# Performance work log

Hardware: AMD Instinct MI355X
Metric: run time of the kernel (lower is better)

The kernel has to match this reference:

```python
import jax, jax.numpy as jnp
import numpy as np

DIM = 1024
NUM_HEADS = 16
HEAD_DIM = DIM // NUM_HEADS
MAX_LEN = 2048
ROPE_BASE = 10000.0


def _rope_tables(n, d, base=ROPE_BASE):
    inv_freq = 1.0 / (base ** (np.arange(0, d, 2, dtype=np.float32) / d))  # [d/2]
    t = np.arange(n, dtype=np.float32)
    freqs = np.outer(t, inv_freq)  # [n, d/2]
    return jnp.asarray(np.cos(freqs)), jnp.asarray(np.sin(freqs))


def _apply_rotary(x, cos, sin):
    # x: [B, H, N, D]; pairs are consecutive elements (2i, 2i+1)
    xe = x[..., 0::2]
    xo = x[..., 1::2]
    # cos/sin: [N, D/2] -> broadcast over B, H
    oe = xe * cos - xo * sin
    oo = xe * sin + xo * cos
    return jnp.stack([oe, oo], axis=-1).reshape(x.shape)


def setup_inputs() -> dict:
    key = jax.random.key(0)
    ks = jax.random.split(key, 11)
    B, T, S = 4, 2048, 2048
    sc = 1.0 / np.sqrt(DIM)
    inp = {
        "query": jax.random.normal(ks[0], (B, T, DIM), jnp.float32),
        "key": jax.random.normal(ks[1], (B, S, DIM), jnp.float32),
        "value": jax.random.normal(ks[2], (B, S, DIM), jnp.float32),
        "Wq": jax.random.normal(ks[3], (DIM, DIM), jnp.float32) * sc,
        "bq": jnp.zeros((DIM,), jnp.float32),
        "Wk": jax.random.normal(ks[4], (DIM, DIM), jnp.float32) * sc,
        "bk": jnp.zeros((DIM,), jnp.float32),
        "Wv": jax.random.normal(ks[5], (DIM, DIM), jnp.float32) * sc,
        "bv": jnp.zeros((DIM,), jnp.float32),
        "Wo": jax.random.normal(ks[6], (DIM, DIM), jnp.float32) * sc,
        "bo": jnp.zeros((DIM,), jnp.float32),
    }
    return inp


def reference(query, key, value, Wq, bq, Wk, bk, Wv, bv, Wo, bo):
    B, T, C = query.shape
    S = key.shape[1]
    H, D = NUM_HEADS, HEAD_DIM
    scale = D ** -0.5

    q = (query @ Wq + bq).reshape(B, T, H, D).transpose(0, 2, 1, 3)  # [B,H,T,D]
    k = (key @ Wk + bk).reshape(B, S, H, D).transpose(0, 2, 1, 3)    # [B,H,S,D]
    v = (value @ Wv + bv).reshape(B, S, H, D).transpose(0, 2, 1, 3)  # [B,H,S,D]

    cos, sin = _rope_tables(max(T, S), D)
    q = _apply_rotary(q, cos[:T], sin[:T])
    k = _apply_rotary(k, cos[:S], sin[:S])

    scores = jnp.einsum("bhtd,bhsd->bhts", q, k) * scale  # [B,H,T,S]
    causal = jnp.tril(jnp.ones((T, S), bool))
    scores = jnp.where(causal[None, None], scores, -jnp.inf)
    att = jax.nn.softmax(scores, axis=-1)

    out = jnp.einsum("bhts,bhsd->bhtd", att, v)  # [B,H,T,D]
    out = out.transpose(0, 2, 1, 3).reshape(B, T, C)
    return out @ Wo + bo
```

## Files before the change

### kernel.cpp

```cpp
#include <hip/hip_runtime.h>
#include <cstdint>
#include <math.h>

typedef __bf16 bf16_t;
typedef __bf16 bf16x8 __attribute__((ext_vector_type(8)));
typedef __bf16 bf16x4 __attribute__((ext_vector_type(4)));
typedef float f32x4 __attribute__((ext_vector_type(4)));

#define MFMA16(a, b, c) __builtin_amdgcn_mfma_f32_16x16x32_bf16((a), (b), (c), 0, 0, 0)

static constexpr int BATCH = 4;
static constexpr int SEQ = 2048;
static constexpr int DIMC = 1024;
static constexpr int NH = 16;
static constexpr int HD = 64;

__device__ __forceinline__ void async_copy16(void* lds, const void* g) {
    __builtin_amdgcn_global_load_lds(
        (const __attribute__((address_space(1))) void*)g,
        (__attribute__((address_space(3))) void*)lds, 16, 0, 0);
}

__device__ __forceinline__ float fast_exp2(float x) {
#if __has_builtin(__builtin_amdgcn_exp2f)
    return __builtin_amdgcn_exp2f(x);
#else
    return __expf(x * 0.6931471805599453f);
#endif
}

__global__ __launch_bounds__(256) void cvt3(const float* __restrict__ q,
                                            const float* __restrict__ k,
                                            const float* __restrict__ v,
                                            bf16_t* __restrict__ out) {
    const float* in = (blockIdx.y == 0) ? q : ((blockIdx.y == 1) ? k : v);
    bf16_t* o = out + (size_t)blockIdx.y * BATCH * SEQ * DIMC;
    const int i = blockIdx.x * 256 + threadIdx.x;
    const float4 f0 = ((const float4*)in)[i * 2];
    const float4 f1 = ((const float4*)in)[i * 2 + 1];
    bf16x8 vv;
    vv[0] = (bf16_t)f0.x; vv[1] = (bf16_t)f0.y; vv[2] = (bf16_t)f0.z; vv[3] = (bf16_t)f0.w;
    vv[4] = (bf16_t)f1.x; vv[5] = (bf16_t)f1.y; vv[6] = (bf16_t)f1.z; vv[7] = (bf16_t)f1.w;
    ((bf16x8*)o)[i] = vv;
}

__global__ __launch_bounds__(256) void transpose_cvt(const float* __restrict__ W0,
                                                     const float* __restrict__ W1,
                                                     const float* __restrict__ W2,
                                                     const float* __restrict__ W3,
                                                     bf16_t* __restrict__ out) {
    const float* Ws[4] = {W0, W1, W2, W3};
    const float* W = Ws[blockIdx.z];
    bf16_t* Wt = out + (size_t)blockIdx.z * DIMC * DIMC;
    __shared__ float tile[32][33];
    const int tx = threadIdx.x & 31;
    const int ty = threadIdx.x >> 5;
    const int x0 = blockIdx.x * 32;
    const int y0 = blockIdx.y * 32;
    #pragma unroll
    for (int j = ty; j < 32; j += 8)
        tile[j][tx] = W[(size_t)(y0 + j) * DIMC + x0 + tx];
    __syncthreads();
    #pragma unroll
    for (int j = ty; j < 32; j += 8)
        Wt[(size_t)(x0 + j) * DIMC + y0 + tx] = (bf16_t)tile[tx][j];
}

__global__ __launch_bounds__(256) void rope_tab(float* __restrict__ cosT, float* __restrict__ sinT) {
    const int idx = blockIdx.x * 256 + threadIdx.x;
    const int t = idx >> 5;
    const int p = idx & 31;
    const float inv = exp2f(-0.41524101186092029f * (float)p);
    const float ang = (float)t * inv;
    float s, c;
    sincosf(ang, &s, &c);
    cosT[idx] = c;
    sinT[idx] = s;
}

template <int MI>
__device__ __forceinline__ void gemm_core(const bf16_t* __restrict__ A,
                                          const bf16_t* __restrict__ Bt,
                                          const int row0, const int col0,
                                          bf16_t* As, bf16_t* Bs, const int tid,
                                          f32x4 (&acc)[MI][4]) {
    constexpr int ABUF = MI * 32 * 32;
    constexpr int BBUF = 256 * 32;
    constexpr int NT = DIMC / 32;
    const int wid = tid >> 6;
    const int lane = tid & 63;
    const int l15 = lane & 15;
    const int quad = lane >> 4;
    const int wr = wid >> 2;
    const int wc = wid & 3;
    const int rIn = lane >> 2;
    const int gW = ((lane & 3) ^ ((rIn & 3) ^ ((rIn >> 2) & 3))) * 8;
    const int fR = (l15 & 3) ^ ((l15 >> 2) & 3);

#define STAGE_TILE(bi, kt)                                                              \
    {                                                                                   \
        const int k0_ = (kt)*32;                                                        \
        bf16_t* as_ = As + (bi)*ABUF;                                                   \
        bf16_t* bs_ = Bs + (bi)*BBUF;                                                   \
        if constexpr (MI == 8) {                                                        \
            _Pragma("unroll") for (int ci = 0; ci < 2; ++ci) {                          \
                const int c = 2 * wid + ci;                                             \
                async_copy16(&as_[c * 512],                                             \
                             A + (size_t)(row0 + c * 16 + rIn) * DIMC + k0_ + gW);      \
            }                                                                           \
        } else {                                                                        \
            async_copy16(&as_[wid * 512],                                               \
                         A + (size_t)(row0 + wid * 16 + rIn) * DIMC + k0_ + gW);        \
        }                                                                               \
        _Pragma("unroll") for (int ci = 0; ci < 2; ++ci) {                              \
            const int c = 2 * wid + ci;                                                 \
            async_copy16(&bs_[c * 512],                                                 \
                         Bt + (size_t)(col0 + c * 16 + rIn) * DIMC + k0_ + gW);         \
        }                                                                               \
    }

    STAGE_TILE(0, 0)
    STAGE_TILE(1, 1)
    int rb = 0;
    for (int t = 0; t < NT; ++t) {
        if (t == NT - 1) {
            asm volatile("s_waitcnt vmcnt(0)" ::: "memory");
        } else {
            if constexpr (MI == 8)
                asm volatile("s_waitcnt vmcnt(4)" ::: "memory");
            else
                asm volatile("s_waitcnt vmcnt(3)" ::: "memory");
        }
        asm volatile("s_barrier" ::: "memory");
        if (t + 2 < NT) {
            int sb = rb + 2;
            if (sb >= 3) sb -= 3;
            STAGE_TILE(sb, t + 2)
        }
        const bf16_t* as = As + rb * ABUF;
        const bf16_t* bs = Bs + rb * BBUF;
        bf16x8 bfrag[4];
        #pragma unroll
        for (int ni = 0; ni < 4; ++ni)
            bfrag[ni] = *(const bf16x8*)&bs[(wc * 64 + ni * 16 + l15) * 32 + ((quad ^ fR) << 3)];
        bf16x8 afrag[MI];
        #pragma unroll
        for (int mi = 0; mi < MI; ++mi)
            afrag[mi] =
                *(const bf16x8*)&as[(wr * (MI * 16) + mi * 16 + l15) * 32 + ((quad ^ fR) << 3)];
        __builtin_amdgcn_s_setprio(1);
        #pragma unroll
        for (int mi = 0; mi < MI; ++mi)
            #pragma unroll
            for (int ni = 0; ni < 4; ++ni)
                acc[mi][ni] = MFMA16(afrag[mi], bfrag[ni], acc[mi][ni]);
        __builtin_amdgcn_s_setprio(0);
        rb = rb + 1 == 3 ? 0 : rb + 1;
    }
#undef STAGE_TILE
}

__global__ __launch_bounds__(512, 2) void gemm_qkv(const bf16_t* __restrict__ Cb,
                                                   const bf16_t* __restrict__ Wt3,
                                                   const float* __restrict__ bq,
                                                   const float* __restrict__ bk,
                                                   const float* __restrict__ bv,
                                                   bf16_t* __restrict__ Qr,
                                                   bf16_t* __restrict__ Kr,
                                                   bf16_t* __restrict__ Vr,
                                                   const float* __restrict__ cosT,
                                                   const float* __restrict__ sinT) {
    __shared__ __align__(16) unsigned char smem[98304];
    bf16_t* As = (bf16_t*)smem;
    bf16_t* Bs = (bf16_t*)(smem + 49152);
    float* eps = (float*)smem;
    const int z = blockIdx.z;
    const bf16_t* A = Cb + (size_t)z * BATCH * SEQ * DIMC;
    const bf16_t* Bt = Wt3 + (size_t)z * DIMC * DIMC;
    const float* bias = (z == 0) ? bq : ((z == 1) ? bk : bv);
    bf16_t* outp = (z == 0) ? Qr : ((z == 1) ? Kr : Vr);
    const bool rope = (z < 2);
    const int tid = threadIdx.x;
    const int row0 = blockIdx.y * 256, col0 = blockIdx.x * 256;
    f32x4 acc[8][4] = {};
    gemm_core<8>(A, Bt, row0, col0, As, Bs, tid, acc);

    const int wid = tid >> 6;
    const int lane = tid & 63;
    const int l15 = lane & 15;
    const int quad = lane >> 4;
    const int wr = wid >> 2, wc = wid & 3;
    float bvl[4];
    #pragma unroll
    for (int ni = 0; ni < 4; ++ni) bvl[ni] = bias[col0 + wc * 64 + ni * 16 + l15];
    const int lr = tid >> 4;
    const int cg = tid & 15;
    const int c0 = cg * 16;
    const int h = (col0 + c0) >> 6;
    const int dbase = c0 & 63;
    const float osc = (z == 0) ? 0.18033688011112043f : 1.0f;
    #pragma unroll
    for (int p = 0; p < 8; ++p) {
        __syncthreads();
        #pragma unroll
        for (int ni = 0; ni < 4; ++ni)
            #pragma unroll
            for (int r = 0; r < 4; ++r)
                eps[(wr * 16 + quad * 4 + r) * 264 + wc * 64 + ni * 16 + l15] =
                    acc[p][ni][r] + bvl[ni];
        __syncthreads();
        const int grow = row0 + (lr >> 4) * 128 + p * 16 + (lr & 15);
        const int tq = grow & (SEQ - 1);
        const int bb = grow >> 11;
        float vals[16];
        #pragma unroll
        for (int q4 = 0; q4 < 4; ++q4) {
            f32x4 vv = *(const f32x4*)&eps[lr * 264 + c0 + q4 * 4];
            vals[q4 * 4 + 0] = vv[0]; vals[q4 * 4 + 1] = vv[1];
            vals[q4 * 4 + 2] = vv[2]; vals[q4 * 4 + 3] = vv[3];
        }
        bf16x8 o0, o1;
        if (rope) {
            const int pbase = tq * 32 + (dbase >> 1);
            const float4 cs0 = *(const float4*)&cosT[pbase];
            const float4 cs1 = *(const float4*)&cosT[pbase + 4];
            const float4 sn0 = *(const float4*)&sinT[pbase];
            const float4 sn1 = *(const float4*)&sinT[pbase + 4];
            const float cc[8] = {cs0.x, cs0.y, cs0.z, cs0.w, cs1.x, cs1.y, cs1.z, cs1.w};
            const float ss[8] = {sn0.x, sn0.y, sn0.z, sn0.w, sn1.x, sn1.y, sn1.z, sn1.w};
            #pragma unroll
            for (int i = 0; i < 8; ++i) {
                const float e = vals[2 * i], o = vals[2 * i + 1];
                const float oe = (e * cc[i] - o * ss[i]) * osc;
                const float oo = (e * ss[i] + o * cc[i]) * osc;
                if (i < 4) { o0[2 * i] = (bf16_t)oe; o0[2 * i + 1] = (bf16_t)oo; }
                else { o1[2 * (i - 4)] = (bf16_t)oe; o1[2 * (i - 4) + 1] = (bf16_t)oo; }
            }
        } else {
            #pragma unroll
            for (int i = 0; i < 8; ++i) o0[i] = (bf16_t)vals[i];
            #pragma unroll
            for (int i = 0; i < 8; ++i) o1[i] = (bf16_t)vals[8 + i];
        }
        bf16_t* dst = outp + (((size_t)bb * NH + h) * SEQ + tq) * HD + dbase;
        *(bf16x8*)dst = o0;
        *(bf16x8*)(dst + 8) = o1;
    }
}

__global__ __launch_bounds__(512, 2) void gemm_o(const bf16_t* __restrict__ A,
                                                 const bf16_t* __restrict__ Bt,
                                                 const float* __restrict__ bias,
                                                 float* __restrict__ out) {
    __shared__ __align__(16) unsigned char smem[73728];
    bf16_t* As = (bf16_t*)smem;
    bf16_t* Bs = (bf16_t*)(smem + 24576);
    const int tid = threadIdx.x;
    const int row0 = blockIdx.y * 128, col0 = blockIdx.x * 256;
    f32x4 acc[4][4] = {};
    gemm_core<4>(A, Bt, row0, col0, As, Bs, tid, acc);
    const int wid = tid >> 6;
    const int lane = tid & 63;
    const int l15 = lane & 15;
    const int quad = lane >> 4;
    const int wr = wid >> 2, wc = wid & 3;
    #pragma unroll
    for (int ni = 0; ni < 4; ++ni) {
        const int col = col0 + wc * 64 + ni * 16 + l15;
        const float bvl = bias[col];
        #pragma unroll
        for (int mi = 0; mi < 4; ++mi) {
            #pragma unroll
            for (int r = 0; r < 4; ++r) {
                const int row = row0 + wr * 64 + mi * 16 + quad * 4 + r;
                out[(size_t)row * DIMC + col] = acc[mi][ni][r] + bvl;
            }
        }
    }
}

__global__ __launch_bounds__(256) void attn_kernel(const bf16_t* __restrict__ Qr,
                                                   const bf16_t* __restrict__ Kr,
                                                   const bf16_t* __restrict__ Vr,
                                                   bf16_t* __restrict__ O) {
    __shared__ bf16_t Ks[2][64 * 64];
    __shared__ bf16_t Vt[2][64 * 72];
    __shared__ bf16_t Ps[4][32 * 72];
    const int tid = threadIdx.x;
    const int w = tid >> 6;
    const int lane = tid & 63;
    const int l15 = lane & 15;
    const int quad = lane >> 4;
    const int bh = blockIdx.x;
    const int b = bh >> 4, h = bh & 15;
    const bf16_t* Qb = Qr + (size_t)bh * SEQ * HD;
    const bf16_t* Kb = Kr + (size_t)bh * SEQ * HD;
    const bf16_t* Vb = Vr + (size_t)bh * SEQ * HD;

    bf16x8 ones;
    #pragma unroll
    for (int j8 = 0; j8 < 8; ++j8) ones[j8] = (bf16_t)1.0f;
    bf16x8 idB[2];
    #pragma unroll
    for (int ch = 0; ch < 2; ++ch)
        #pragma unroll
        for (int j8 = 0; j8 < 8; ++j8)
            idB[ch][j8] = (quad * 8 + j8 == ch * 16 + l15) ? (bf16_t)1.0f : (bf16_t)0.0f;

    const int sIn = lane >> 3;
    const int gK = ((lane & 7) ^ sIn) * 8;
    const int fK = (l15 & 7);

#define VTRANS(buf, a0, a1)                                                      \
    {                                                                            \
        _Pragma("unroll") for (int c = 0; c < 4; ++c) {                          \
            f32x4 zt = {};                                                       \
            f32x4 tv = MFMA16((c < 2) ? (a0) : (a1), idB[c & 1], zt);            \
            bf16x4 pkt;                                                          \
            _Pragma("unroll") for (int rr = 0; rr < 4; ++rr)                     \
                pkt[rr] = (bf16_t)tv[rr];                                        \
            *(bf16x4*)&Vt[buf][(c * 16 + l15) * 72 + w * 16 + quad * 4] = pkt;   \
        }                                                                        \
    }

    const int j = 15 - (int)blockIdx.y;
    const int q0 = j * 128;
    bf16x8 qa[2][2];
    #pragma unroll
    for (int mg = 0; mg < 2; ++mg)
        #pragma unroll
        for (int kc = 0; kc < 2; ++kc)
            qa[mg][kc] = *(const bf16x8*)(Qb + (size_t)(q0 + mg * 64 + w * 16 + l15) * HD +
                                          kc * 32 + quad * 8);
    f32x4 acco[2][4] = {};
    f32x4 accl[2] = {};
    const int nIter = 2 * j + 2;

    #pragma unroll
    for (int ci = 0; ci < 2; ++ci) {
        const int c = 2 * w + ci;
        async_copy16(&Ks[0][c * 512], Kb + (size_t)(c * 8 + sIn) * HD + gK);
    }
    {
        const bf16_t* vsrc = Vb + (size_t)(w * 16 + l15) * HD + quad * 8;
        bf16x8 pv0 = *(const bf16x8*)vsrc;
        bf16x8 pv1 = *(const bf16x8*)(vsrc + 32);
        VTRANS(0, pv0, pv1);
    }
    __syncthreads();

    int cur = 0;
    for (int it = 0; it < nIter; ++it) {
        const int nxt = cur ^ 1;
        const bool hn = (it + 1 < nIter);
        bf16x8 av0, av1;
        if (hn) {
            const int s1 = (it + 1) * 64;
            #pragma unroll
            for (int ci = 0; ci < 2; ++ci) {
                const int c = 2 * w + ci;
                async_copy16(&Ks[nxt][c * 512], Kb + (size_t)(s1 + c * 8 + sIn) * HD + gK);
            }
            const bf16_t* vsrc = Vb + (size_t)(s1 + w * 16 + l15) * HD + quad * 8;
            av0 = *(const bf16x8*)vsrc;
            av1 = *(const bf16x8*)(vsrc + 32);
        }
        bf16x8 kb[4][2];
        #pragma unroll
        for (int mt = 0; mt < 4; ++mt)
            #pragma unroll
            for (int kc = 0; kc < 2; ++kc)
                kb[mt][kc] = *(const bf16x8*)&Ks[cur][(mt * 16 + l15) * 64 +
                                                      (((kc * 4 + quad) ^ fK) << 3)];
        const bool skip0 = (it == 2 * j + 1);
        f32x4 zz[2][4];
        __builtin_amdgcn_s_setprio(1);
        #pragma unroll
        for (int mg = 0; mg < 2; ++mg) {
            if (mg == 0 && skip0) continue;
            #pragma unroll
            for (int mt = 0; mt < 4; ++mt) {
                f32x4 z = {};
                z = MFMA16(kb[mt][0], qa[mg][0], z);
                z = MFMA16(kb[mt][1], qa[mg][1], z);
                zz[mg][mt] = z;
            }
        }
        __builtin_amdgcn_s_setprio(0);
        #pragma unroll
        for (int mg = 0; mg < 2; ++mg) {
            if (mg == 0 && skip0) continue;
            const bool diag = (it == 2 * j + mg);
            #pragma unroll
            for (int mt = 0; mt < 4; ++mt) {
                bf16x4 pk;
                #pragma unroll
                for (int r = 0; r < 4; ++r) {
                    float v = zz[mg][mt][r];
                    if (diag && (mt * 16 + quad * 4 + r > w * 16 + l15)) v = -INFINITY;
                    pk[r] = (bf16_t)fast_exp2(v);
                }
                *(bf16x4*)&Ps[w][(mg * 16 + l15) * 72 + mt * 16 + quad * 4] = pk;
            }
        }
        asm volatile("s_waitcnt lgkmcnt(0)" ::: "memory");
        bf16x8 vb[4][2];
        #pragma unroll
        for (int dt = 0; dt < 4; ++dt)
            #pragma unroll
            for (int kc = 0; kc < 2; ++kc)
                vb[dt][kc] = *(const bf16x8*)&Vt[cur][(dt * 16 + l15) * 72 + kc * 32 + quad * 8];
        #pragma unroll
        for (int mg = 0; mg < 2; ++mg) {
            if (mg == 0 && skip0) continue;
            const bf16x8 pa0 = *(const bf16x8*)&Ps[w][(mg * 16 + l15) * 72 + quad * 8];
            const bf16x8 pa1 = *(const bf16x8*)&Ps[w][(mg * 16 + l15) * 72 + 32 + quad * 8];
            __builtin_amdgcn_s_setprio(1);
            #pragma unroll
            for (int dt = 0; dt < 4; ++dt) {
                acco[mg][dt] = MFMA16(pa0, vb[dt][0], acco[mg][dt]);
                acco[mg][dt] = MFMA16(pa1, vb[dt][1], acco[mg][dt]);
            }
            accl[mg] = MFMA16(pa0, ones, accl[mg]);
            accl[mg] = MFMA16(pa1, ones, accl[mg]);
            __builtin_amdgcn_s_setprio(0);
        }
        if (hn) VTRANS(nxt, av0, av1);
        __syncthreads();
        cur = nxt;
    }
    #pragma unroll
    for (int mg = 0; mg < 2; ++mg) {
        #pragma unroll
        for (int r = 0; r < 4; ++r) {
            const float inv = 1.0f / accl[mg][r];
            const int trow = q0 + mg * 64 + w * 16 + quad * 4 + r;
            bf16_t* orow = O + ((size_t)(b * SEQ + trow)) * DIMC + h * HD;
            #pragma unroll
            for (int dt = 0; dt < 4; ++dt)
                orow[dt * 16 + l15] = (bf16_t)(acco[mg][dt][r] * inv);
        }
    }
#undef VTRANS
}

extern "C" void kernel_launch(void* const* d_in, const int* in_sizes, int n_in,
                              void* d_out, int out_size, void* d_ws, size_t ws_size,
                              hipStream_t stream) {
    const float* query = (const float*)d_in[0];
    const float* key = (const float*)d_in[1];
    const float* value = (const float*)d_in[2];
    const float* Wq = (const float*)d_in[3];
    const float* bq = (const float*)d_in[4];
    const float* Wk = (const float*)d_in[5];
    const float* bk = (const float*)d_in[6];
    const float* Wv = (const float*)d_in[7];
    const float* bv = (const float*)d_in[8];
    const float* Wo = (const float*)d_in[9];
    const float* bo = (const float*)d_in[10];

    char* ws = (char*)d_ws;
    const size_t WT_BYTES = (size_t)DIMC * DIMC * sizeof(bf16_t);
    const size_t ACT_BYTES = (size_t)BATCH * SEQ * DIMC * sizeof(bf16_t);
    bf16_t* WT = (bf16_t*)ws;
    bf16_t* WoT = WT + 3 * (size_t)DIMC * DIMC;
    float* cosT = (float*)(ws + 4 * WT_BYTES);
    float* sinT = (float*)(ws + 4 * WT_BYTES + 262144);
    bf16_t* Cb = (bf16_t*)(ws + 4 * WT_BYTES + 2 * 262144);
    bf16_t* Qr = (bf16_t*)((char*)Cb + 3 * ACT_BYTES);
    bf16_t* Kr = (bf16_t*)((char*)Cb + 4 * ACT_BYTES);
    bf16_t* Vr = (bf16_t*)((char*)Cb + 5 * ACT_BYTES);
    bf16_t* Ob = Cb;

    transpose_cvt<<<dim3(32, 32, 4), 256, 0, stream>>>(Wq, Wk, Wv, Wo, WT);
    rope_tab<<<dim3(256), 256, 0, stream>>>(cosT, sinT);
    cvt3<<<dim3(4096, 3), 256, 0, stream>>>(query, key, value, Cb);
    gemm_qkv<<<dim3(DIMC / 256, (BATCH * SEQ) / 256, 3), 512, 0, stream>>>(
        Cb, WT, bq, bk, bv, Qr, Kr, Vr, cosT, sinT);
    attn_kernel<<<dim3(BATCH * NH, 16), 256, 0, stream>>>(Qr, Kr, Vr, Ob);
    gemm_o<<<dim3(DIMC / 256, (BATCH * SEQ) / 128), 512, 0, stream>>>(Ob, WoT, bo, (float*)d_out);
}
```

Measured before the change: 332.5 us.

## Rewrite GEMM core with 64-wide K tiles and split-phase pipelined staging

```diff
diff --git a/kernel.cpp b/kernel.cpp
--- a/kernel.cpp
+++ b/kernel.cpp
@@ -78,86 +78,94 @@
     sinT[idx] = s;
 }
 
-template <int MI>
-__device__ __forceinline__ void gemm_core(const bf16_t* __restrict__ A,
-                                          const bf16_t* __restrict__ Bt,
-                                          const int row0, const int col0,
-                                          bf16_t* As, bf16_t* Bs, const int tid,
-                                          f32x4 (&acc)[MI][4]) {
-    constexpr int ABUF = MI * 32 * 32;
-    constexpr int BBUF = 256 * 32;
-    constexpr int NT = DIMC / 32;
+__device__ __forceinline__ void gemm_core64(const bf16_t* __restrict__ A,
+                                            const bf16_t* __restrict__ Bt,
+                                            const int row0, const int col0,
+                                            bf16_t* As, bf16_t* Bs, const int tid,
+                                            f32x4 (&acc)[4][4]) {
+    constexpr int NT = DIMC / 64;
     const int wid = tid >> 6;
     const int lane = tid & 63;
     const int l15 = lane & 15;
     const int quad = lane >> 4;
     const int wr = wid >> 2;
     const int wc = wid & 3;
-    const int rIn = lane >> 2;
-    const int gW = ((lane & 3) ^ ((rIn & 3) ^ ((rIn >> 2) & 3))) * 8;
-    const int fR = (l15 & 3) ^ ((l15 >> 2) & 3);
-
-#define STAGE_TILE(bi, kt)                                                              \
-    {                                                                                   \
-        const int k0_ = (kt)*32;                                                        \
-        bf16_t* as_ = As + (bi)*ABUF;                                                   \
-        bf16_t* bs_ = Bs + (bi)*BBUF;                                                   \
-        if constexpr (MI == 8) {                                                        \
-            _Pragma("unroll") for (int ci = 0; ci < 2; ++ci) {                          \
-                const int c = 2 * wid + ci;                                             \
-                async_copy16(&as_[c * 512],                                             \
-                             A + (size_t)(row0 + c * 16 + rIn) * DIMC + k0_ + gW);      \
-            }                                                                           \
-        } else {                                                                        \
-            async_copy16(&as_[wid * 512],                                               \
-                         A + (size_t)(row0 + wid * 16 + rIn) * DIMC + k0_ + gW);        \
-        }                                                                               \
-        _Pragma("unroll") for (int ci = 0; ci < 2; ++ci) {                              \
-            const int c = 2 * wid + ci;                                                 \
-            async_copy16(&bs_[c * 512],                                                 \
-                         Bt + (size_t)(col0 + c * 16 + rIn) * DIMC + k0_ + gW);         \
-        }                                                                               \
-    }
-
-    STAGE_TILE(0, 0)
-    STAGE_TILE(1, 1)
+    const int rL = tid >> 3;
+    const int gswE = ((tid & 7) ^ (rL & 7)) * 8;
+    const int e0 = ((quad) ^ (l15 & 7)) * 8;
+    const int e1 = ((4 + quad) ^ (l15 & 7)) * 8;
+    const int aRow = wr * 64 + l15;
+    const int bRow = wc * 64 + l15;
+
+#define STG_A64(bi, kt, p)                                                     \
+    async_copy16(As + (bi)*8192 + (p)*4096 + tid * 8,                          \
+                 A + (size_t)(row0 + (p)*64 + rL) * DIMC + (kt)*64 + gswE);
+#define STG_B64(bi, kt, p)                                                     \
+    async_copy16(Bs + (bi)*16384 + (p)*4096 + tid * 8,                         \
+                 Bt + (size_t)(col0 + (p)*64 + rL) * DIMC + (kt)*64 + gswE);
+
+    STG_A64(0, 0, 0) STG_A64(0, 0, 1)
+    STG_B64(0, 0, 0) STG_B64(0, 0, 1) STG_B64(0, 0, 2) STG_B64(0, 0, 3)
+    STG_A64(1, 1, 0) STG_A64(1, 1, 1)
+    STG_B64(1, 1, 0) STG_B64(1, 1, 1) STG_B64(1, 1, 2) STG_B64(1, 1, 3)
+    asm volatile("s_waitcnt vmcnt(6)" ::: "memory");
+    __builtin_amdgcn_s_barrier();
+
     int rb = 0;
+    #pragma unroll 1
     for (int t = 0; t < NT; ++t) {
-        if (t == NT - 1) {
+        int sb = rb + 2;
+        if (sb >= 3) sb -= 3;
+        const int kt2 = t + 2;
+        const bool st = kt2 < NT;
+        const bf16_t* as = As + rb * 8192;
+        const bf16_t* bs = Bs + rb * 16384;
+        bf16x8 af[4], bf[4];
+        #pragma unroll
+        for (int mi = 0; mi < 4; ++mi)
+            af[mi] = *(const bf16x8*)&as[(aRow + mi * 16) * 64 + e0];
+        #pragma unroll
+        for (int ni = 0; ni < 4; ++ni)
+            bf[ni] = *(const bf16x8*)&bs[(bRow + ni * 16) * 64 + e0];
+        if (st) { STG_A64(sb, kt2, 0) STG_A64(sb, kt2, 1) STG_B64(sb, kt2, 0) }
+        __builtin_amdgcn_s_barrier();
+        asm volatile("s_waitcnt lgkmcnt(0)" ::: "memory");
+        __builtin_amdgcn_sched_barrier(0);
+        __builtin_amdgcn_s_setprio(1);
+        #pragma unroll
+        for (int mi = 0; mi < 4; ++mi)
+            #pragma unroll
+            for (int ni = 0; ni < 4; ++ni)
+                acc[mi][ni] = MFMA16(af[mi], bf[ni], acc[mi][ni]);
+        __builtin_amdgcn_s_setprio(0);
+        __builtin_amdgcn_s_barrier();
+        #pragma unroll
+        for (int mi = 0; mi < 4; ++mi)
+            af[mi] = *(const bf16x8*)&as[(aRow + mi * 16) * 64 + e1];
+        #pragma unroll
+        for (int ni = 0; ni < 4; ++ni)
+            bf[ni] = *(const bf16x8*)&bs[(bRow + ni * 16) * 64 + e1];
+        if (st) { STG_B64(sb, kt2, 1) STG_B64(sb, kt2, 2) STG_B64(sb, kt2, 3) }
+        __builtin_amdgcn_s_barrier();
+        asm volatile("s_waitcnt lgkmcnt(0)" ::: "memory");
+        __builtin_amdgcn_sched_barrier(0);
+        __builtin_amdgcn_s_setprio(1);
+        #pragma unroll
+        for (int mi = 0; mi < 4; ++mi)
+            #pragma unroll
+            for (int ni = 0; ni < 4; ++ni)
+                acc[mi][ni] = MFMA16(af[mi], bf[ni], acc[mi][ni]);
+        __builtin_amdgcn_s_setprio(0);
+        if (t < NT - 2)
+            asm volatile("s_waitcnt vmcnt(6)" ::: "memory");
+        else
             asm volatile("s_waitcnt vmcnt(0)" ::: "memory");
-        } else {
-            if constexpr (MI == 8)
-                asm volatile("s_waitcnt vmcnt(4)" ::: "memory");
-            else
-                asm volatile("s_waitcnt vmcnt(3)" ::: "memory");
-        }
-        asm volatile("s_barrier" ::: "memory");
-        if (t + 2 < NT) {
-            int sb = rb + 2;
-            if (sb >= 3) sb -= 3;
-            STAGE_TILE(sb, t + 2)
-        }
-        const bf16_t* as = As + rb * ABUF;
-        const bf16_t* bs = Bs + rb * BBUF;
-        bf16x8 bfrag[4];
-        #pragma unroll
-        for (int ni = 0; ni < 4; ++ni)
-            bfrag[ni] = *(const bf16x8*)&bs[(wc * 64 + ni * 16 + l15) * 32 + ((quad ^ fR) << 3)];
-        bf16x8 afrag[MI];
-        #pragma unroll
-        for (int mi = 0; mi < MI; ++mi)
-            afrag[mi] =
-                *(const bf16x8*)&as[(wr * (MI * 16) + mi * 16 + l15) * 32 + ((quad ^ fR) << 3)];
-        __builtin_amdgcn_s_setprio(1);
-        #pragma unroll
-        for (int mi = 0; mi < MI; ++mi)
-            #pragma unroll
-            for (int ni = 0; ni < 4; ++ni)
-                acc[mi][ni] = MFMA16(afrag[mi], bfrag[ni], acc[mi][ni]);
-        __builtin_amdgcn_s_setprio(0);
-        rb = rb + 1 == 3 ? 0 : rb + 1;
-    }
-#undef STAGE_TILE
+        __builtin_amdgcn_s_barrier();
+        rb = rb + 1;
+        if (rb >= 3) rb = 0;
+    }
+#undef STG_A64
+#undef STG_B64
 }
 
 __global__ __launch_bounds__(512, 2) void gemm_qkv(const bf16_t* __restrict__ Cb,
@@ -170,7 +178,7 @@
                                                    bf16_t* __restrict__ Vr,
                                                    const float* __restrict__ cosT,
                                                    const float* __restrict__ sinT) {
-    __shared__ __align__(16) unsigned char smem[98304];
+    __shared__ __align__(16) unsigned char smem[147456];
     bf16_t* As = (bf16_t*)smem;
     bf16_t* Bs = (bf16_t*)(smem + 49152);
     float* eps = (float*)smem;
@@ -181,9 +189,9 @@
     bf16_t* outp = (z == 0) ? Qr : ((z == 1) ? Kr : Vr);
     const bool rope = (z < 2);
     const int tid = threadIdx.x;
-    const int row0 = blockIdx.y * 256, col0 = blockIdx.x * 256;
-    f32x4 acc[8][4] = {};
-    gemm_core<8>(A, Bt, row0, col0, As, Bs, tid, acc);
+    const int row0 = blockIdx.x * 128, col0 = blockIdx.y * 256;
+    f32x4 acc[4][4] = {};
+    gemm_core64(A, Bt, row0, col0, As, Bs, tid, acc);
 
     const int wid = tid >> 6;
     const int lane = tid & 63;
@@ -200,7 +208,7 @@
     const int dbase = c0 & 63;
     const float osc = (z == 0) ? 0.18033688011112043f : 1.0f;
     #pragma unroll
-    for (int p = 0; p < 8; ++p) {
+    for (int p = 0; p < 4; ++p) {
         __syncthreads();
         #pragma unroll
         for (int ni = 0; ni < 4; ++ni)
@@ -209,7 +217,7 @@
                 eps[(wr * 16 + quad * 4 + r) * 264 + wc * 64 + ni * 16 + l15] =
                     acc[p][ni][r] + bvl[ni];
         __syncthreads();
-        const int grow = row0 + (lr >> 4) * 128 + p * 16 + (lr & 15);
+        const int grow = row0 + (lr >> 4) * 64 + p * 16 + (lr & 15);
         const int tq = grow & (SEQ - 1);
         const int bb = grow >> 11;
         float vals[16];
@@ -252,13 +260,13 @@
                                                  const bf16_t* __restrict__ Bt,
                                                  const float* __restrict__ bias,
                                                  float* __restrict__ out) {
-    __shared__ __align__(16) unsigned char smem[73728];
+    __shared__ __align__(16) unsigned char smem[147456];
     bf16_t* As = (bf16_t*)smem;
-    bf16_t* Bs = (bf16_t*)(smem + 24576);
+    bf16_t* Bs = (bf16_t*)(smem + 49152);
     const int tid = threadIdx.x;
-    const int row0 = blockIdx.y * 128, col0 = blockIdx.x * 256;
+    const int row0 = blockIdx.x * 128, col0 = blockIdx.y * 256;
     f32x4 acc[4][4] = {};
-    gemm_core<4>(A, Bt, row0, col0, As, Bs, tid, acc);
+    gemm_core64(A, Bt, row0, col0, As, Bs, tid, acc);
     const int wid = tid >> 6;
     const int lane = tid & 63;
     const int l15 = lane & 15;
@@ -475,8 +483,8 @@
     transpose_cvt<<<dim3(32, 32, 4), 256, 0, stream>>>(Wq, Wk, Wv, Wo, WT);
     rope_tab<<<dim3(256), 256, 0, stream>>>(cosT, sinT);
     cvt3<<<dim3(4096, 3), 256, 0, stream>>>(query, key, value, Cb);
-    gemm_qkv<<<dim3(DIMC / 256, (BATCH * SEQ) / 256, 3), 512, 0, stream>>>(
+    gemm_qkv<<<dim3((BATCH * SEQ) / 128, DIMC / 256, 3), 512, 0, stream>>>(
         Cb, WT, bq, bk, bv, Qr, Kr, Vr, cosT, sinT);
     attn_kernel<<<dim3(BATCH * NH, 16), 256, 0, stream>>>(Qr, Kr, Vr, Ob);
-    gemm_o<<<dim3(DIMC / 256, (BATCH * SEQ) / 128), 512, 0, stream>>>(Ob, WoT, bo, (float*)d_out);
-}
+    gemm_o<<<dim3((BATCH * SEQ) / 128, DIMC / 256), 512, 0, stream>>>(Ob, WoT, bo, (float*)d_out);
+}
```

Measured after the change: 318.6 us. 1.04x faster.
